# Performance work log

Measured on AMD Instinct MI355X. Metric: run time of the kernel, lower is better.

The kernel has to match this reference:

```python
import jax, jax.numpy as jnp
import numpy as np
from math import factorial, sqrt

L_MAX = 3
MUL = 64
# e3nn FullyConnectedTensorProduct instruction order: lexicographic over (l1, l2, l3)
# keeping paths with triangle inequality and matching parity ((-1)^(l1+l2) == (-1)^l3).
PATHS = [(l1, l2, l3)
         for l1 in range(L_MAX + 1)
         for l2 in range(L_MAX + 1)
         for l3 in range(L_MAX + 1)
         if abs(l1 - l2) <= l3 <= l1 + l2 and (l1 + l2 + l3) % 2 == 0]
assert len(PATHS) == 23
N_TO = {l3: sum(1 for p in PATHS if p[2] == l3) for l3 in range(L_MAX + 1)}


def _su2_cg(j1, m1, j2, m2, j3, m3):
    # Complex-basis Clebsch-Gordan coefficient (Racah formula), as in e3nn.
    if m3 != m1 + m2:
        return 0.0
    f = factorial
    vmin = max(-j1 + j2 + m3, -j1 + m1, 0)
    vmax = min(j2 + j3 + m1, j3 - j1 + j2, j3 + m3)
    c = sqrt((2 * j3 + 1) * f(j3 + j1 - j2) * f(j3 - j1 + j2) * f(j1 + j2 - j3)
             * f(j3 + m3) * f(j3 - m3)
             / (f(j1 + j2 + j3 + 1) * f(j1 - m1) * f(j1 + m1) * f(j2 - m2) * f(j2 + m2)))
    s = 0.0
    for v in range(vmin, vmax + 1):
        s += (-1) ** (v + j2 + m2) / f(v) * f(j2 + j3 + m1 - v) * f(j1 - m1 + v) \
             / f(j3 - j1 + j2 - v) / f(j3 + m3 - v) / f(v + j1 - j2 - m3)
    return c * s


def _q(l):
    # Change of basis real -> complex spherical harmonics (e3nn convention).
    q = np.zeros((2 * l + 1, 2 * l + 1), dtype=np.complex128)
    for m in range(-l, 0):
        q[l + m, l + abs(m)] = 1.0 / np.sqrt(2.0)
        q[l + m, l - abs(m)] = -1j / np.sqrt(2.0)
    q[l, l] = 1.0
    for m in range(1, l + 1):
        q[l + m, l + abs(m)] = (-1) ** m / np.sqrt(2.0)
        q[l + m, l - abs(m)] = 1j * (-1) ** m / np.sqrt(2.0)
    return (-1j) ** l * q


def _w3j(l1, l2, l3):
    # Real-basis Wigner 3j tensor, unit Frobenius norm (e3nn's o3.wigner_3j).
    csu2 = np.zeros((2 * l1 + 1, 2 * l2 + 1, 2 * l3 + 1))
    for m1 in range(-l1, l1 + 1):
        for m2 in range(-l2, l2 + 1):
            m3 = m1 + m2
            if -l3 <= m3 <= l3:
                csu2[l1 + m1, l2 + m2, l3 + m3] = _su2_cg(l1, m1, l2, m2, l3, m3)
    q1, q2, q3 = _q(l1), _q(l2), _q(l3)
    c = np.einsum('ij,kl,mn,ikn->jlm', q1, q2, np.conj(q3.T), csu2.astype(np.complex128))
    c = np.real(c)
    return (c / np.linalg.norm(c)).astype(np.float32)


W3J = {p: jnp.asarray(_w3j(*p)) for p in PATHS}
# e3nn 'component' irrep_normalization + 'element' path_normalization:
# per-path coeff = sqrt(ir_out.dim / (n_paths_into_out * mul1 * mul2)).
COEFF = {p: float(np.sqrt((2 * p[2] + 1) / (N_TO[p[2]] * MUL * MUL))) for p in PATHS}


def setup_inputs():
    key = jax.random.key(0)
    kx, kw = jax.random.split(key)
    x = jax.random.normal(kx, (2, 1024, MUL * (L_MAX + 1) ** 2), dtype=jnp.float32)
    weights = jax.random.normal(kw, (len(PATHS), MUL, MUL, MUL), dtype=jnp.float32)
    return {"x": x, "weights": weights}


def reference(x, weights):
    B, N, D = x.shape
    Z = B * N
    xf = x.reshape(Z, D)
    # e3nn layout: blocks of (mul, 2l+1) concatenated over l; offset = MUL * l^2.
    xs = [xf[:, MUL * l * l: MUL * (l + 1) ** 2].reshape(Z, MUL, 2 * l + 1)
          for l in range(L_MAX + 1)]
    acc = [jnp.zeros((Z, MUL, 2 * l + 1), dtype=x.dtype) for l in range(L_MAX + 1)]
    for p, (l1, l2, l3) in enumerate(PATHS):
        c = W3J[(l1, l2, l3)]
        t1 = jnp.einsum('zui,ijk->zujk', xs[l1], c)            # [Z,u,2l2+1,2l3+1]
        t2 = jnp.einsum('zujk,zvj->zuvk', t1, xs[l2])          # [Z,u,v,2l3+1]
        seg = jnp.einsum('zuvk,uvw->zwk', t2, weights[p]) * COEFF[(l1, l2, l3)]
        acc[l3] = acc[l3] + seg
    out = jnp.concatenate([a.reshape(Z, -1) for a in acc], axis=-1)
    return out.reshape(B, N, -1)
```

## Files before the change

kernel.cpp:

```cpp
#include <hip/hip_runtime.h>

struct CD { double re, im; };
constexpr CD cmul(CD a, CD b){ return CD{a.re*b.re - a.im*b.im, a.re*b.im + a.im*b.re}; }
constexpr CD conj_(CD a){ return CD{a.re, -a.im}; }

constexpr double factd(int n){ double r = 1.0; for(int i = 2; i <= n; ++i) r *= (double)i; return r; }
constexpr double csqrt_(double x){
  if (x <= 0.0) return 0.0;
  double g = x > 1.0 ? x : 1.0;
  for (int i = 0; i < 100; ++i) g = 0.5*(g + x/g);
  return g;
}

constexpr double su2_cg(int j1,int m1,int j2,int m2,int j3,int m3){
  if (m3 != m1 + m2) return 0.0;
  int vmin = -j1 + j2 + m3;
  if (-j1 + m1 > vmin) vmin = -j1 + m1;
  if (0 > vmin) vmin = 0;
  int vmax = j2 + j3 + m1;
  if (j3 - j1 + j2 < vmax) vmax = j3 - j1 + j2;
  if (j3 + m3 < vmax) vmax = j3 + m3;
  double c = csqrt_((2.0*j3 + 1.0) * factd(j3 + j1 - j2) * factd(j3 - j1 + j2) * factd(j1 + j2 - j3)
                    * factd(j3 + m3) * factd(j3 - m3)
                    / (factd(j1 + j2 + j3 + 1) * factd(j1 - m1) * factd(j1 + m1)
                       * factd(j2 - m2) * factd(j2 + m2)));
  double s = 0.0;
  for (int v = vmin; v <= vmax; ++v){
    double t = (((v + j2 + m2) & 1) ? -1.0 : 1.0) / factd(v)
               * factd(j2 + j3 + m1 - v) * factd(j1 - m1 + v)
               / factd(j3 - j1 + j2 - v) / factd(j3 + m3 - v) / factd(v + j1 - j2 - m3);
    s += t;
  }
  return c * s;
}

struct QM { CD m[7][7]; };
constexpr QM qmat(int l){
  QM q{};
  double is2 = 1.0 / csqrt_(2.0);
  for (int mm = -l; mm < 0; ++mm){
    q.m[l+mm][l-mm] = CD{is2, 0.0};
    q.m[l+mm][l+mm] = CD{0.0, -is2};
  }
  q.m[l][l] = CD{1.0, 0.0};
  for (int mm = 1; mm <= l; ++mm){
    double sgn = (mm & 1) ? -1.0 : 1.0;
    q.m[l+mm][l+mm] = CD{sgn*is2, 0.0};
    q.m[l+mm][l-mm] = CD{0.0, sgn*is2};
  }
  CD ph = (l % 4 == 0) ? CD{1,0} : (l % 4 == 1) ? CD{0,-1} : (l % 4 == 2) ? CD{-1,0} : CD{0,1};
  for (int r = 0; r < 7; ++r)
    for (int c = 0; c < 7; ++c)
      q.m[r][c] = cmul(ph, q.m[r][c]);
  return q;
}

template<int L1,int L2,int L3> struct W3JT { float v[2*L1+1][2*L2+1][2*L3+1]; };

template<int L1,int L2,int L3>
constexpr W3JT<L1,L2,L3> make_w3j(){
  constexpr int D1 = 2*L1+1, D2 = 2*L2+1, D3 = 2*L3+1;
  QM q1 = qmat(L1), q2 = qmat(L2), q3 = qmat(L3);
  double cg[7][7] = {};
  for (int i = 0; i < D1; ++i)
    for (int k = 0; k < D2; ++k){
      int n = i + k - L1 - L2 + L3;
      if (n >= 0 && n < D3) cg[i][k] = su2_cg(L1, i-L1, L2, k-L2, L3, (i-L1)+(k-L2));
    }
  double c[D1][D2][D3] = {};
  double norm2 = 0.0;
  for (int j = 0; j < D1; ++j)
    for (int l = 0; l < D2; ++l)
      for (int m = 0; m < D3; ++m){
        CD s{0.0, 0.0};
        for (int i = 0; i < D1; ++i)
          for (int k = 0; k < D2; ++k){
            double g = cg[i][k];
            if (g == 0.0) continue;
            int n = i + k - L1 - L2 + L3;
            CD t = cmul(q1.m[i][j], q2.m[k][l]);
            t = cmul(t, conj_(q3.m[n][m]));
            s.re += t.re * g; s.im += t.im * g;
          }
        c[j][l][m] = s.re;
        norm2 += s.re * s.re;
      }
  double inv = 1.0 / csqrt_(norm2);
  W3JT<L1,L2,L3> w{};
  for (int j = 0; j < D1; ++j)
    for (int l = 0; l < D2; ++l)
      for (int m = 0; m < D3; ++m){
        double val = c[j][l][m] * inv;
        if (val < 1e-10 && val > -1e-10) val = 0.0;
        w.v[j][l][m] = (float)val;
      }
  return w;
}

__device__ __constant__ int L3P_[23]  = {0,1,2,3,1,0,2,1,3,2,2,1,3,0,2,1,3,3,2,1,3,0,2};
__device__ __constant__ int SWAPP_[23] = {0,1,1,1,0,0,0,1,1,1,0,0,0,0,0,1,1,0,0,0,0,0,0};
constexpr int K3CUM[24] = {0,1,4,9,16,19,20,25,28,35,40,45,48,55,56,61,64,71,78,83,86,93,94,99};
constexpr size_t PSLICE = 2048ull * 64ull;

typedef __bf16 bf16x8 __attribute__((ext_vector_type(8)));
typedef float  f32x4  __attribute__((ext_vector_type(4)));
typedef float  f32x2  __attribute__((ext_vector_type(2)));

__global__ void pack_w_kernel(const float* __restrict__ w, unsigned short* __restrict__ wp, int total){
  int idx = blockIdx.x * 256 + threadIdx.x;
  if (idx >= total) return;
  int e    = idx & 7;
  int lane = (idx >> 3) & 63;
  int nt   = (idx >> 9) & 3;
  int hf   = (idx >> 11) & 1;
  int s    = (idx >> 12) & 63;
  int p    = idx >> 18;
  int kv = hf*32 + (lane >> 4)*8 + e;
  int wc = nt*16 + (lane & 15);
  int l3 = L3P_[p];
  const float nto[4] = {4.f, 6.f, 7.f, 6.f};
  float coeff = sqrtf((2.f*l3 + 1.f) / (nto[l3] * 4096.f));
  int a = SWAPP_[p] ? kv : s;
  int b = SWAPP_[p] ? s : kv;
  float val = w[(((size_t)p*64 + a)*64 + b)*64 + wc] * coeff;
  unsigned bits = __builtin_bit_cast(unsigned, val);
  unsigned r = (bits + 0x7FFFu + ((bits >> 16) & 1u)) >> 16;
  wp[idx] = (unsigned short)r;
}

__global__ void transpose_x(const float* __restrict__ x, float* __restrict__ xT){
  __shared__ float t[32][33];
  int bx = blockIdx.x, by = blockIdx.y;
  int tx = threadIdx.x & 31, ty = threadIdx.x >> 5;
  #pragma unroll
  for (int r = 0; r < 4; ++r)
    t[ty + r*8][tx] = x[(size_t)(by*32 + ty + r*8)*1024 + bx*32 + tx];
  __syncthreads();
  #pragma unroll
  for (int r = 0; r < 4; ++r)
    xT[(size_t)(bx*32 + ty + r*8)*2048 + by*32 + tx] = t[tx][ty + r*8];
}

template<int P,int L1,int L2,int L3,bool SWAP,int G0,int G,bool PART>
__device__ __forceinline__ void run_slot(
    int tile, const float* __restrict__ xT,
    const unsigned short* __restrict__ wp,
    float* __restrict__ dst, float* lds)
{
  constexpr int K3 = 2*L3+1;
  constexpr int LK = SWAP ? L1 : L2;
  constexpr int LS = SWAP ? L2 : L1;
  constexpr int DK = 2*LK+1, DS = 2*LS+1;
  constexpr auto C = make_w3j<L1,L2,L3>();

  const int lane = threadIdx.x & 63;
  const int wv   = threadIdx.x >> 6;
  const int zc   = tile*16 + (lane & 15);
  float* red = lds;
  float* tl  = lds + 3072 + wv*1040;

  f32x2 xk2[4][DK];
  {
    const float* xkb = xT + (size_t)(64*LK*LK)*2048 + zc;
    const int t0 = wv*32 + (lane >> 4)*8;
    #pragma unroll
    for (int q = 0; q < 4; ++q)
      #pragma unroll
      for (int t = 0; t < DK; ++t){
        float lo = xkb[(size_t)((t0 + 2*q    )*DK + t)*2048];
        float hi = xkb[(size_t)((t0 + 2*q + 1)*DK + t)*2048];
        xk2[q][t] = f32x2{lo, hi};
      }
  }

  const float* xsp = xT + (size_t)(64*LS*LS)*2048 + zc;
  const unsigned short* wu = wp + (size_t)P*262144 + (size_t)wv*2048 + (size_t)lane*8;

  f32x4 acc[G][4];
  #pragma unroll
  for (int a = 0; a < G; ++a)
    #pragma unroll
    for (int b = 0; b < 4; ++b) acc[a][b] = f32x4{0.f,0.f,0.f,0.f};

  auto compute = [&](const bf16x8 (&bf)[4], const float (&xs)[DS]){
    #pragma unroll
    for (int kk = 0; kk < G; ++kk){
      float dk[DK];
      #pragma unroll
      for (int t = 0; t < DK; ++t) dk[t] = 0.f;
      #pragma unroll
      for (int t = 0; t < DK; ++t){
        #pragma unroll
        for (int j = 0; j < DS; ++j){
          const float cv = SWAP ? C.v[t][j][G0+kk] : C.v[j][t][G0+kk];
          if (cv != 0.0f) dk[t] = __builtin_fmaf(xs[j], cv, dk[t]);
        }
      }
      f32x2 af2[4];
      #pragma unroll
      for (int q = 0; q < 4; ++q) af2[q] = f32x2{0.f, 0.f};
      #pragma unroll
      for (int t = 0; t < DK; ++t){
        const f32x2 d2 = f32x2{dk[t], dk[t]};
        #pragma unroll
        for (int q = 0; q < 4; ++q)
          af2[q] += xk2[q][t] * d2;
      }
      bf16x8 af;
      #pragma unroll
      for (int q = 0; q < 4; ++q){
        af[2*q]   = (__bf16)af2[q].x;
        af[2*q+1] = (__bf16)af2[q].y;
      }
      __builtin_amdgcn_s_setprio(1);
      #pragma unroll
      for (int nt = 0; nt < 4; ++nt)
        acc[kk][nt] = __builtin_amdgcn_mfma_f32_16x16x32_bf16(af, bf[nt], acc[kk][nt], 0, 0, 0);
      __builtin_amdgcn_s_setprio(0);
    }
  };

  bf16x8 bA[4], bB[4];
  float xs[DS], xn[DS];
  #pragma unroll
  for (int nt = 0; nt < 4; ++nt)
    bA[nt] = *reinterpret_cast<const bf16x8*>(wu + nt*512);
  #pragma unroll
  for (int j = 0; j < DS; ++j) xs[j] = xsp[(size_t)j*2048];

  #pragma unroll 1
  for (int s = 0; s < 64; s += 2){
    #pragma unroll
    for (int nt = 0; nt < 4; ++nt)
      bB[nt] = *reinterpret_cast<const bf16x8*>(wu + 4096 + nt*512);
    #pragma unroll
    for (int j = 0; j < DS; ++j) xn[j] = xsp[(size_t)(DS + j)*2048];

    compute(bA, xs);

    #pragma unroll
    for (int nt = 0; nt < 4; ++nt)
      bA[nt] = *reinterpret_cast<const bf16x8*>(wu + 8192 + nt*512);
    #pragma unroll
    for (int j = 0; j < DS; ++j) xs[j] = xsp[(size_t)(2*DS + j)*2048];

    compute(bB, xn);

    wu  += 8192;
    xsp += (size_t)2*DS*2048;
  }

  constexpr int Gh = (G + 1) / 2;
  static_assert(Gh <= 3, "red[] sized for Gh<=3");
  auto store_kk = [&](int kk, const f32x4 (&sum)[4]){
    if constexpr (PART){
      #pragma unroll
      for (int nt = 0; nt < 4; ++nt)
        #pragma unroll
        for (int r = 0; r < 4; ++r)
          tl[(((lane >> 4)*4 + r))*65 + nt*16 + (lane & 15)] = sum[nt][r];
      #pragma unroll
      for (int zr = 0; zr < 16; ++zr){
        float v = tl[zr*65 + lane];
        dst[(size_t)K3CUM[P]*PSLICE + ((size_t)(tile*16 + zr)*K3 + (G0+kk))*64 + lane] = v;
      }
    } else {
      #pragma unroll
      for (int nt = 0; nt < 4; ++nt)
        #pragma unroll
        for (int r = 0; r < 4; ++r){
          int zl = ((lane >> 4) << 2) + r;
          int wc = nt*16 + (lane & 15);
          unsafeAtomicAdd(dst + (size_t)(tile*16 + zl)*1024 + 64*L3*L3 + wc*K3 + (G0+kk),
                          sum[nt][r]);
        }
    }
  };

  if (wv == 1){
    #pragma unroll
    for (int kk = 0; kk < Gh; ++kk)
      #pragma unroll
      for (int nt = 0; nt < 4; ++nt)
        *reinterpret_cast<f32x4*>(&red[((kk*4 + nt)*64 + lane)*4]) = acc[kk][nt];
  }
  __syncthreads();
  if (wv == 0){
    #pragma unroll
    for (int kk = 0; kk < Gh; ++kk){
      f32x4 sum[4];
      #pragma unroll
      for (int nt = 0; nt < 4; ++nt){
        f32x4 o = *reinterpret_cast<const f32x4*>(&red[((kk*4 + nt)*64 + lane)*4]);
        sum[nt] = acc[kk][nt] + o;
      }
      store_kk(kk, sum);
    }
  }
  if constexpr (G > Gh){
    if (wv == 0){
      #pragma unroll
      for (int kk = Gh; kk < G; ++kk)
        #pragma unroll
        for (int nt = 0; nt < 4; ++nt)
          *reinterpret_cast<f32x4*>(&red[(((kk-Gh)*4 + nt)*64 + lane)*4]) = acc[kk][nt];
    }
    __syncthreads();
    if (wv == 1){
      #pragma unroll
      for (int kk = Gh; kk < G; ++kk){
        f32x4 sum[4];
        #pragma unroll
        for (int nt = 0; nt < 4; ++nt){
          f32x4 o = *reinterpret_cast<const f32x4*>(&red[(((kk-Gh)*4 + nt)*64 + lane)*4]);
          sum[nt] = acc[kk][nt] + o;
        }
        store_kk(kk, sum);
      }
    }
  }
}

template<bool PART>
__global__ __launch_bounds__(128, 3) void tp_main(const float* __restrict__ xT,
    const unsigned short* __restrict__ wp, float* __restrict__ dst)
{
  __shared__ __align__(16) float lds[5152];
  const int slot = blockIdx.x >> 7;
  const int tile = blockIdx.x & 127;
  switch (slot){
    case 0:  run_slot<16,2,3,3,true ,0,2,PART>(tile,xT,wp,dst,lds); break;
    case 1:  run_slot<16,2,3,3,true ,2,2,PART>(tile,xT,wp,dst,lds); break;
    case 2:  run_slot<16,2,3,3,true ,4,2,PART>(tile,xT,wp,dst,lds); break;
    case 3:  run_slot<16,2,3,3,true ,6,1,PART>(tile,xT,wp,dst,lds); break;
    case 4:  run_slot<20,3,2,3,false,0,2,PART>(tile,xT,wp,dst,lds); break;
    case 5:  run_slot<20,3,2,3,false,2,2,PART>(tile,xT,wp,dst,lds); break;
    case 6:  run_slot<20,3,2,3,false,4,2,PART>(tile,xT,wp,dst,lds); break;
    case 7:  run_slot<20,3,2,3,false,6,1,PART>(tile,xT,wp,dst,lds); break;
    case 8:  run_slot<22,3,3,2,false,0,1,PART>(tile,xT,wp,dst,lds); break;
    case 9:  run_slot<22,3,3,2,false,1,1,PART>(tile,xT,wp,dst,lds); break;
    case 10: run_slot<22,3,3,2,false,2,1,PART>(tile,xT,wp,dst,lds); break;
    case 11: run_slot<22,3,3,2,false,3,1,PART>(tile,xT,wp,dst,lds); break;
    case 12: run_slot<22,3,3,2,false,4,1,PART>(tile,xT,wp,dst,lds); break;
    case 13: run_slot<14,2,2,2,false,0,2,PART>(tile,xT,wp,dst,lds); break;
    case 14: run_slot<14,2,2,2,false,2,2,PART>(tile,xT,wp,dst,lds); break;
    case 15: run_slot<14,2,2,2,false,4,1,PART>(tile,xT,wp,dst,lds); break;
    case 16: run_slot< 8,1,2,3,true ,0,3,PART>(tile,xT,wp,dst,lds); break;
    case 17: run_slot< 8,1,2,3,true ,3,3,PART>(tile,xT,wp,dst,lds); break;
    case 18: run_slot< 8,1,2,3,true ,6,1,PART>(tile,xT,wp,dst,lds); break;
    case 19: run_slot<12,2,1,3,false,0,3,PART>(tile,xT,wp,dst,lds); break;
    case 20: run_slot<12,2,1,3,false,3,3,PART>(tile,xT,wp,dst,lds); break;
    case 21: run_slot<12,2,1,3,false,6,1,PART>(tile,xT,wp,dst,lds); break;
    case 22: run_slot<15,2,3,1,true ,0,2,PART>(tile,xT,wp,dst,lds); break;
    case 23: run_slot<15,2,3,1,true ,2,1,PART>(tile,xT,wp,dst,lds); break;
    case 24: run_slot<19,3,2,1,false,0,2,PART>(tile,xT,wp,dst,lds); break;
    case 25: run_slot<19,3,2,1,false,2,1,PART>(tile,xT,wp,dst,lds); break;
    case 26: run_slot< 6,1,1,2,false,0,3,PART>(tile,xT,wp,dst,lds); break;
    case 27: run_slot< 6,1,1,2,false,3,2,PART>(tile,xT,wp,dst,lds); break;
    case 28: run_slot< 9,1,3,2,true ,0,3,PART>(tile,xT,wp,dst,lds); break;
    case 29: run_slot< 9,1,3,2,true ,3,2,PART>(tile,xT,wp,dst,lds); break;
    case 30: run_slot<18,3,1,2,false,0,3,PART>(tile,xT,wp,dst,lds); break;
    case 31: run_slot<18,3,1,2,false,3,2,PART>(tile,xT,wp,dst,lds); break;
    case 32: run_slot< 7,1,2,1,true ,0,3,PART>(tile,xT,wp,dst,lds); break;
    case 33: run_slot<11,2,1,1,false,0,3,PART>(tile,xT,wp,dst,lds); break;
    case 34: run_slot<21,3,3,0,false,0,1,PART>(tile,xT,wp,dst,lds); break;
    case 35: run_slot<13,2,2,0,false,0,1,PART>(tile,xT,wp,dst,lds); break;
    case 36: run_slot< 3,0,3,3,true ,0,3,PART>(tile,xT,wp,dst,lds); break;
    case 37: run_slot< 3,0,3,3,true ,3,3,PART>(tile,xT,wp,dst,lds); break;
    case 38: run_slot< 3,0,3,3,true ,6,1,PART>(tile,xT,wp,dst,lds); break;
    case 39: run_slot<17,3,0,3,false,0,3,PART>(tile,xT,wp,dst,lds); break;
    case 40: run_slot<17,3,0,3,false,3,3,PART>(tile,xT,wp,dst,lds); break;
    case 41: run_slot<17,3,0,3,false,6,1,PART>(tile,xT,wp,dst,lds); break;
    case 42: run_slot< 2,0,2,2,true ,0,3,PART>(tile,xT,wp,dst,lds); break;
    case 43: run_slot< 2,0,2,2,true ,3,2,PART>(tile,xT,wp,dst,lds); break;
    case 44: run_slot<10,2,0,2,false,0,3,PART>(tile,xT,wp,dst,lds); break;
    case 45: run_slot<10,2,0,2,false,3,2,PART>(tile,xT,wp,dst,lds); break;
    case 46: run_slot< 1,0,1,1,true ,0,3,PART>(tile,xT,wp,dst,lds); break;
    case 47: run_slot< 4,1,0,1,false,0,3,PART>(tile,xT,wp,dst,lds); break;
    case 48: run_slot< 5,1,1,0,false,0,1,PART>(tile,xT,wp,dst,lds); break;
    case 49: run_slot< 0,0,0,0,false,0,1,PART>(tile,xT,wp,dst,lds); break;
    default: break;
  }
}

__global__ void gather_out(const float* __restrict__ part, float* __restrict__ out){
  const int z = blockIdx.x;
  const int t = threadIdx.x;
  const int w = t & 63;
  const int g = t >> 6;
  float* ob = out + (size_t)z*1024;
  auto rd = [&](int p, int K3p, int k){
    return part[(size_t)K3CUM[p]*PSLICE + ((size_t)z*K3p + k)*64 + w];
  };
  if (g == 0){
    ob[w] = rd(0,1,0) + rd(5,1,0) + rd(13,1,0) + rd(21,1,0);
  } else if (g == 1){
    #pragma unroll
    for (int k = 0; k < 3; ++k)
      ob[64 + w*3 + k] = rd(1,3,k) + rd(4,3,k) + rd(7,3,k)
                       + rd(11,3,k) + rd(15,3,k) + rd(19,3,k);
  } else if (g == 2){
    #pragma unroll
    for (int k = 0; k < 5; ++k)
      ob[256 + w*5 + k] = rd(2,5,k) + rd(6,5,k) + rd(9,5,k) + rd(10,5,k)
                        + rd(14,5,k) + rd(18,5,k) + rd(22,5,k);
  } else {
    #pragma unroll
    for (int k = 0; k < 7; ++k)
      ob[576 + w*7 + k] = rd(3,7,k) + rd(8,7,k) + rd(12,7,k)
                        + rd(16,7,k) + rd(17,7,k) + rd(20,7,k);
  }
}

extern "C" void kernel_launch(void* const* d_in, const int* in_sizes, int n_in,
                              void* d_out, int out_size, void* d_ws, size_t ws_size,
                              hipStream_t stream)
{
  const float* x = (const float*)d_in[0];
  const float* w = (const float*)d_in[1];
  float* out = (float*)d_out;

  const size_t packB = 23ull*64*2*4*64*8 * sizeof(unsigned short);
  const size_t xTB   = 1024ull*2048*sizeof(float);
  const size_t partB = 99ull*PSLICE*sizeof(float);
  const size_t slack = 131072;
  const int totalW = 23*64*2*4*64*8;

  unsigned short* wp = (unsigned short*)d_ws;
  float* xT   = (float*)((char*)d_ws + packB);
  float* part = (float*)((char*)d_ws + packB + xTB);

  if (ws_size < packB + xTB + slack) return;

  pack_w_kernel<<<(totalW + 255)/256, 256, 0, stream>>>(w, wp, totalW);
  dim3 tg(32, 64);
  transpose_x<<<tg, 256, 0, stream>>>(x, xT);

  if (ws_size >= packB + xTB + partB + slack){
    tp_main<true><<<50*128, 128, 0, stream>>>(xT, wp, part);
    gather_out<<<2048, 256, 0, stream>>>(part, out);
  } else {
    hipMemsetAsync(d_out, 0, (size_t)out_size * sizeof(float), stream);
    tp_main<false><<<50*128, 128, 0, stream>>>(xT, wp, out);
  }
}
```

Before: 212.0 us.

## Precontract W3J with loop-invariant x operand for low-l paths and regroup slots

Adds a YKS mode that precomputes, once per block, the contraction of the register-held x operand with the Wigner-3j coefficients (yk), so the inner loop only needs a DS-wide FMA per k instead of a two-stage contraction. For small-l paths the swap choice is flipped so the smaller irrep is streamed. Slot groupings are rebalanced to 55 slots with different G splits. This trades more registers for the yk array, which may lower occupancy, for fewer per-iteration VALU ops.

After: 231.0 us. +9.0%, slower.

```diff
diff --git a/kernel.cpp b/kernel.cpp
--- a/kernel.cpp
+++ b/kernel.cpp
@@ -98,7 +98,7 @@
 }
 
 __device__ __constant__ int L3P_[23]  = {0,1,2,3,1,0,2,1,3,2,2,1,3,0,2,1,3,3,2,1,3,0,2};
-__device__ __constant__ int SWAPP_[23] = {0,1,1,1,0,0,0,1,1,1,0,0,0,0,0,1,1,0,0,0,0,0,0};
+__device__ __constant__ int SWAPP_[23] = {1,0,0,0,1,1,1,0,0,0,1,1,1,0,0,1,1,1,1,0,0,0,0};
 constexpr int K3CUM[24] = {0,1,4,9,16,19,20,25,28,35,40,45,48,55,56,61,64,71,78,83,86,93,94,99};
 constexpr size_t PSLICE = 2048ull * 64ull;
 
@@ -141,7 +141,7 @@
     xT[(size_t)(bx*32 + ty + r*8)*2048 + by*32 + tx] = t[tx][ty + r*8];
 }
 
-template<int P,int L1,int L2,int L3,bool SWAP,int G0,int G,bool PART>
+template<int P,int L1,int L2,int L3,bool SWAP,bool YKS,int G0,int G,bool PART>
 __device__ __forceinline__ void run_slot(
     int tile, const float* __restrict__ xT,
     const unsigned short* __restrict__ wp,
@@ -159,18 +159,46 @@
   float* red = lds;
   float* tl  = lds + 3072 + wv*1040;
 
+  f32x2 yk[G][4][DS];
   f32x2 xk2[4][DK];
   {
     const float* xkb = xT + (size_t)(64*LK*LK)*2048 + zc;
     const int t0 = wv*32 + (lane >> 4)*8;
-    #pragma unroll
-    for (int q = 0; q < 4; ++q)
+    if constexpr (YKS){
+      #pragma unroll
+      for (int kk = 0; kk < G; ++kk)
+        #pragma unroll
+        for (int q = 0; q < 4; ++q)
+          #pragma unroll
+          for (int j = 0; j < DS; ++j) yk[kk][q][j] = f32x2{0.f, 0.f};
       #pragma unroll
       for (int t = 0; t < DK; ++t){
-        float lo = xkb[(size_t)((t0 + 2*q    )*DK + t)*2048];
-        float hi = xkb[(size_t)((t0 + 2*q + 1)*DK + t)*2048];
-        xk2[q][t] = f32x2{lo, hi};
-      }
+        f32x2 xt[4];
+        #pragma unroll
+        for (int q = 0; q < 4; ++q)
+          xt[q] = f32x2{ xkb[(size_t)((t0 + 2*q    )*DK + t)*2048],
+                         xkb[(size_t)((t0 + 2*q + 1)*DK + t)*2048] };
+        #pragma unroll
+        for (int kk = 0; kk < G; ++kk)
+          #pragma unroll
+          for (int j = 0; j < DS; ++j){
+            const float cv = SWAP ? C.v[t][j][G0+kk] : C.v[j][t][G0+kk];
+            if (cv != 0.0f){
+              const f32x2 c2 = f32x2{cv, cv};
+              #pragma unroll
+              for (int q = 0; q < 4; ++q)
+                yk[kk][q][j] += xt[q] * c2;
+            }
+          }
+      }
+    } else {
+      #pragma unroll
+      for (int q = 0; q < 4; ++q)
+        #pragma unroll
+        for (int t = 0; t < DK; ++t)
+          xk2[q][t] = f32x2{ xkb[(size_t)((t0 + 2*q    )*DK + t)*2048],
+                             xkb[(size_t)((t0 + 2*q + 1)*DK + t)*2048] };
+    }
   }
 
   const float* xsp = xT + (size_t)(64*LS*LS)*2048 + zc;
@@ -185,26 +213,36 @@
   auto compute = [&](const bf16x8 (&bf)[4], const float (&xs)[DS]){
     #pragma unroll
     for (int kk = 0; kk < G; ++kk){
-      float dk[DK];
-      #pragma unroll
-      for (int t = 0; t < DK; ++t) dk[t] = 0.f;
-      #pragma unroll
-      for (int t = 0; t < DK; ++t){
+      f32x2 af2[4];
+      #pragma unroll
+      for (int q = 0; q < 4; ++q) af2[q] = f32x2{0.f, 0.f};
+      if constexpr (YKS){
         #pragma unroll
         for (int j = 0; j < DS; ++j){
-          const float cv = SWAP ? C.v[t][j][G0+kk] : C.v[j][t][G0+kk];
-          if (cv != 0.0f) dk[t] = __builtin_fmaf(xs[j], cv, dk[t]);
+          const f32x2 d2 = f32x2{xs[j], xs[j]};
+          #pragma unroll
+          for (int q = 0; q < 4; ++q)
+            af2[q] += yk[kk][q][j] * d2;
         }
-      }
-      f32x2 af2[4];
-      #pragma unroll
-      for (int q = 0; q < 4; ++q) af2[q] = f32x2{0.f, 0.f};
-      #pragma unroll
-      for (int t = 0; t < DK; ++t){
-        const f32x2 d2 = f32x2{dk[t], dk[t]};
-        #pragma unroll
-        for (int q = 0; q < 4; ++q)
-          af2[q] += xk2[q][t] * d2;
+      } else {
+        float dk[DK];
+        #pragma unroll
+        for (int t = 0; t < DK; ++t) dk[t] = 0.f;
+        #pragma unroll
+        for (int t = 0; t < DK; ++t){
+          #pragma unroll
+          for (int j = 0; j < DS; ++j){
+            const float cv = SWAP ? C.v[t][j][G0+kk] : C.v[j][t][G0+kk];
+            if (cv != 0.0f) dk[t] = __builtin_fmaf(xs[j], cv, dk[t]);
+          }
+        }
+        #pragma unroll
+        for (int t = 0; t < DK; ++t){
+          const f32x2 d2 = f32x2{dk[t], dk[t]};
+          #pragma unroll
+          for (int q = 0; q < 4; ++q)
+            af2[q] += xk2[q][t] * d2;
+        }
       }
       bf16x8 af;
       #pragma unroll
@@ -329,56 +367,61 @@
   const int slot = blockIdx.x >> 7;
   const int tile = blockIdx.x & 127;
   switch (slot){
-    case 0:  run_slot<16,2,3,3,true ,0,2,PART>(tile,xT,wp,dst,lds); break;
-    case 1:  run_slot<16,2,3,3,true ,2,2,PART>(tile,xT,wp,dst,lds); break;
-    case 2:  run_slot<16,2,3,3,true ,4,2,PART>(tile,xT,wp,dst,lds); break;
-    case 3:  run_slot<16,2,3,3,true ,6,1,PART>(tile,xT,wp,dst,lds); break;
-    case 4:  run_slot<20,3,2,3,false,0,2,PART>(tile,xT,wp,dst,lds); break;
-    case 5:  run_slot<20,3,2,3,false,2,2,PART>(tile,xT,wp,dst,lds); break;
-    case 6:  run_slot<20,3,2,3,false,4,2,PART>(tile,xT,wp,dst,lds); break;
-    case 7:  run_slot<20,3,2,3,false,6,1,PART>(tile,xT,wp,dst,lds); break;
-    case 8:  run_slot<22,3,3,2,false,0,1,PART>(tile,xT,wp,dst,lds); break;
-    case 9:  run_slot<22,3,3,2,false,1,1,PART>(tile,xT,wp,dst,lds); break;
-    case 10: run_slot<22,3,3,2,false,2,1,PART>(tile,xT,wp,dst,lds); break;
-    case 11: run_slot<22,3,3,2,false,3,1,PART>(tile,xT,wp,dst,lds); break;
-    case 12: run_slot<22,3,3,2,false,4,1,PART>(tile,xT,wp,dst,lds); break;
-    case 13: run_slot<14,2,2,2,false,0,2,PART>(tile,xT,wp,dst,lds); break;
-    case 14: run_slot<14,2,2,2,false,2,2,PART>(tile,xT,wp,dst,lds); break;
-    case 15: run_slot<14,2,2,2,false,4,1,PART>(tile,xT,wp,dst,lds); break;
-    case 16: run_slot< 8,1,2,3,true ,0,3,PART>(tile,xT,wp,dst,lds); break;
-    case 17: run_slot< 8,1,2,3,true ,3,3,PART>(tile,xT,wp,dst,lds); break;
-    case 18: run_slot< 8,1,2,3,true ,6,1,PART>(tile,xT,wp,dst,lds); break;
-    case 19: run_slot<12,2,1,3,false,0,3,PART>(tile,xT,wp,dst,lds); break;
-    case 20: run_slot<12,2,1,3,false,3,3,PART>(tile,xT,wp,dst,lds); break;
-    case 21: run_slot<12,2,1,3,false,6,1,PART>(tile,xT,wp,dst,lds); break;
-    case 22: run_slot<15,2,3,1,true ,0,2,PART>(tile,xT,wp,dst,lds); break;
-    case 23: run_slot<15,2,3,1,true ,2,1,PART>(tile,xT,wp,dst,lds); break;
-    case 24: run_slot<19,3,2,1,false,0,2,PART>(tile,xT,wp,dst,lds); break;
-    case 25: run_slot<19,3,2,1,false,2,1,PART>(tile,xT,wp,dst,lds); break;
-    case 26: run_slot< 6,1,1,2,false,0,3,PART>(tile,xT,wp,dst,lds); break;
-    case 27: run_slot< 6,1,1,2,false,3,2,PART>(tile,xT,wp,dst,lds); break;
-    case 28: run_slot< 9,1,3,2,true ,0,3,PART>(tile,xT,wp,dst,lds); break;
-    case 29: run_slot< 9,1,3,2,true ,3,2,PART>(tile,xT,wp,dst,lds); break;
-    case 30: run_slot<18,3,1,2,false,0,3,PART>(tile,xT,wp,dst,lds); break;
-    case 31: run_slot<18,3,1,2,false,3,2,PART>(tile,xT,wp,dst,lds); break;
-    case 32: run_slot< 7,1,2,1,true ,0,3,PART>(tile,xT,wp,dst,lds); break;
-    case 33: run_slot<11,2,1,1,false,0,3,PART>(tile,xT,wp,dst,lds); break;
-    case 34: run_slot<21,3,3,0,false,0,1,PART>(tile,xT,wp,dst,lds); break;
-    case 35: run_slot<13,2,2,0,false,0,1,PART>(tile,xT,wp,dst,lds); break;
-    case 36: run_slot< 3,0,3,3,true ,0,3,PART>(tile,xT,wp,dst,lds); break;
-    case 37: run_slot< 3,0,3,3,true ,3,3,PART>(tile,xT,wp,dst,lds); break;
-    case 38: run_slot< 3,0,3,3,true ,6,1,PART>(tile,xT,wp,dst,lds); break;
-    case 39: run_slot<17,3,0,3,false,0,3,PART>(tile,xT,wp,dst,lds); break;
-    case 40: run_slot<17,3,0,3,false,3,3,PART>(tile,xT,wp,dst,lds); break;
-    case 41: run_slot<17,3,0,3,false,6,1,PART>(tile,xT,wp,dst,lds); break;
-    case 42: run_slot< 2,0,2,2,true ,0,3,PART>(tile,xT,wp,dst,lds); break;
-    case 43: run_slot< 2,0,2,2,true ,3,2,PART>(tile,xT,wp,dst,lds); break;
-    case 44: run_slot<10,2,0,2,false,0,3,PART>(tile,xT,wp,dst,lds); break;
-    case 45: run_slot<10,2,0,2,false,3,2,PART>(tile,xT,wp,dst,lds); break;
-    case 46: run_slot< 1,0,1,1,true ,0,3,PART>(tile,xT,wp,dst,lds); break;
-    case 47: run_slot< 4,1,0,1,false,0,3,PART>(tile,xT,wp,dst,lds); break;
-    case 48: run_slot< 5,1,1,0,false,0,1,PART>(tile,xT,wp,dst,lds); break;
-    case 49: run_slot< 0,0,0,0,false,0,1,PART>(tile,xT,wp,dst,lds); break;
+    case 0:  run_slot<16,2,3,3,true ,false,0,2,PART>(tile,xT,wp,dst,lds); break;
+    case 1:  run_slot<16,2,3,3,true ,false,2,2,PART>(tile,xT,wp,dst,lds); break;
+    case 2:  run_slot<16,2,3,3,true ,false,4,2,PART>(tile,xT,wp,dst,lds); break;
+    case 3:  run_slot<16,2,3,3,true ,false,6,1,PART>(tile,xT,wp,dst,lds); break;
+    case 4:  run_slot<20,3,2,3,false,false,0,2,PART>(tile,xT,wp,dst,lds); break;
+    case 5:  run_slot<20,3,2,3,false,false,2,2,PART>(tile,xT,wp,dst,lds); break;
+    case 6:  run_slot<20,3,2,3,false,false,4,2,PART>(tile,xT,wp,dst,lds); break;
+    case 7:  run_slot<20,3,2,3,false,false,6,1,PART>(tile,xT,wp,dst,lds); break;
+    case 8:  run_slot<22,3,3,2,false,false,0,1,PART>(tile,xT,wp,dst,lds); break;
+    case 9:  run_slot<22,3,3,2,false,false,1,1,PART>(tile,xT,wp,dst,lds); break;
+    case 10: run_slot<22,3,3,2,false,false,2,1,PART>(tile,xT,wp,dst,lds); break;
+    case 11: run_slot<22,3,3,2,false,false,3,1,PART>(tile,xT,wp,dst,lds); break;
+    case 12: run_slot<22,3,3,2,false,false,4,1,PART>(tile,xT,wp,dst,lds); break;
+    case 13: run_slot<14,2,2,2,false,false,0,2,PART>(tile,xT,wp,dst,lds); break;
+    case 14: run_slot<14,2,2,2,false,false,2,2,PART>(tile,xT,wp,dst,lds); break;
+    case 15: run_slot<14,2,2,2,false,false,4,1,PART>(tile,xT,wp,dst,lds); break;
+    case 16: run_slot<15,2,3,1,true ,false,0,2,PART>(tile,xT,wp,dst,lds); break;
+    case 17: run_slot<15,2,3,1,true ,false,2,1,PART>(tile,xT,wp,dst,lds); break;
+    case 18: run_slot<19,3,2,1,false,false,0,2,PART>(tile,xT,wp,dst,lds); break;
+    case 19: run_slot<19,3,2,1,false,false,2,1,PART>(tile,xT,wp,dst,lds); break;
+    case 20: run_slot<21,3,3,0,false,false,0,1,PART>(tile,xT,wp,dst,lds); break;
+    case 21: run_slot<13,2,2,0,false,false,0,1,PART>(tile,xT,wp,dst,lds); break;
+    case 22: run_slot< 9,1,3,2,false,true ,0,2,PART>(tile,xT,wp,dst,lds); break;
+    case 23: run_slot< 9,1,3,2,false,true ,2,2,PART>(tile,xT,wp,dst,lds); break;
+    case 24: run_slot< 9,1,3,2,false,true ,4,1,PART>(tile,xT,wp,dst,lds); break;
+    case 25: run_slot<18,3,1,2,true ,true ,0,2,PART>(tile,xT,wp,dst,lds); break;
+    case 26: run_slot<18,3,1,2,true ,true ,2,2,PART>(tile,xT,wp,dst,lds); break;
+    case 27: run_slot<18,3,1,2,true ,true ,4,1,PART>(tile,xT,wp,dst,lds); break;
+    case 28: run_slot< 8,1,2,3,false,true ,0,2,PART>(tile,xT,wp,dst,lds); break;
+    case 29: run_slot< 8,1,2,3,false,true ,2,2,PART>(tile,xT,wp,dst,lds); break;
+    case 30: run_slot< 8,1,2,3,false,true ,4,2,PART>(tile,xT,wp,dst,lds); break;
+    case 31: run_slot< 8,1,2,3,false,true ,6,1,PART>(tile,xT,wp,dst,lds); break;
+    case 32: run_slot<12,2,1,3,true ,true ,0,2,PART>(tile,xT,wp,dst,lds); break;
+    case 33: run_slot<12,2,1,3,true ,true ,2,2,PART>(tile,xT,wp,dst,lds); break;
+    case 34: run_slot<12,2,1,3,true ,true ,4,2,PART>(tile,xT,wp,dst,lds); break;
+    case 35: run_slot<12,2,1,3,true ,true ,6,1,PART>(tile,xT,wp,dst,lds); break;
+    case 36: run_slot< 6,1,1,2,true ,true ,0,2,PART>(tile,xT,wp,dst,lds); break;
+    case 37: run_slot< 6,1,1,2,true ,true ,2,2,PART>(tile,xT,wp,dst,lds); break;
+    case 38: run_slot< 6,1,1,2,true ,true ,4,1,PART>(tile,xT,wp,dst,lds); break;
+    case 39: run_slot< 7,1,2,1,false,true ,0,2,PART>(tile,xT,wp,dst,lds); break;
+    case 40: run_slot< 7,1,2,1,false,true ,2,1,PART>(tile,xT,wp,dst,lds); break;
+    case 41: run_slot<11,2,1,1,true ,true ,0,2,PART>(tile,xT,wp,dst,lds); break;
+    case 42: run_slot<11,2,1,1,true ,true ,2,1,PART>(tile,xT,wp,dst,lds); break;
+    case 43: run_slot< 5,1,1,0,true ,true ,0,1,PART>(tile,xT,wp,dst,lds); break;
+    case 44: run_slot< 3,0,3,3,false,true ,0,4,PART>(tile,xT,wp,dst,lds); break;
+    case 45: run_slot< 3,0,3,3,false,true ,4,3,PART>(tile,xT,wp,dst,lds); break;
+    case 46: run_slot<17,3,0,3,true ,true ,0,4,PART>(tile,xT,wp,dst,lds); break;
+    case 47: run_slot<17,3,0,3,true ,true ,4,3,PART>(tile,xT,wp,dst,lds); break;
+    case 48: run_slot< 2,0,2,2,false,true ,0,4,PART>(tile,xT,wp,dst,lds); break;
+    case 49: run_slot< 2,0,2,2,false,true ,4,1,PART>(tile,xT,wp,dst,lds); break;
+    case 50: run_slot<10,2,0,2,true ,true ,0,4,PART>(tile,xT,wp,dst,lds); break;
+    case 51: run_slot<10,2,0,2,true ,true ,4,1,PART>(tile,xT,wp,dst,lds); break;
+    case 52: run_slot< 1,0,1,1,false,true ,0,3,PART>(tile,xT,wp,dst,lds); break;
+    case 53: run_slot< 4,1,0,1,true ,true ,0,3,PART>(tile,xT,wp,dst,lds); break;
+    case 54: run_slot< 0,0,0,0,true ,true ,0,1,PART>(tile,xT,wp,dst,lds); break;
     default: break;
   }
 }
@@ -437,10 +480,10 @@
   transpose_x<<<tg, 256, 0, stream>>>(x, xT);
 
   if (ws_size >= packB + xTB + partB + slack){
-    tp_main<true><<<50*128, 128, 0, stream>>>(xT, wp, part);
+    tp_main<true><<<55*128, 128, 0, stream>>>(xT, wp, part);
     gather_out<<<2048, 256, 0, stream>>>(part, out);
   } else {
     hipMemsetAsync(d_out, 0, (size_t)out_size * sizeof(float), stream);
-    tp_main<false><<<50*128, 128, 0, stream>>>(xT, wp, out);
-  }
-}
+    tp_main<false><<<55*128, 128, 0, stream>>>(xT, wp, out);
+  }
+}
```
